# Optimization experiments

Measured on AMD Instinct MI355X. Metric: run time of the kernel, lower is better.

## Reference

```python
import jax, jax.numpy as jnp
import numpy as np

SMOOTH_STEP_PARAM = 1.0  # = 1/gamma in the TEL paper
DEPTH = 6


def smooth_step(x):
    # TEL smooth-step: 0 for u<=-1/2, 1 for u>=1/2, cubic -2u^3+1.5u+0.5 inside.
    u = SMOOTH_STEP_PARAM * x
    inner = (-2.0 * u + 1.5) * u * u + (u + 0.5) * 0.0 + (-2.0 * u ** 3 + 1.5 * u + 0.5)
    # use single clean expression for the cubic
    cubic = -2.0 * u ** 3 + 1.5 * u + 0.5
    return jnp.where(u <= -0.5, 0.0, jnp.where(u >= 0.5, 1.0, cubic))


def setup_inputs() -> dict:
    key = jax.random.key(0)
    k1, k2, k3 = jax.random.split(key, 3)
    B, D, T, O = 32768, 1024, 8, 128
    num_leaves = 2 ** DEPTH
    x = jax.random.normal(k1, (B, D), dtype=jnp.float32)
    # RandomUniform(-0.01, 0.01) initializers in the original layer
    node_weights = jax.random.uniform(k2, (T, D, num_leaves - 1), dtype=jnp.float32,
                                      minval=-0.01, maxval=0.01)
    leaf_weights = jax.random.uniform(k3, (T, O, num_leaves), dtype=jnp.float32,
                                      minval=-0.01, maxval=0.01)
    return {"x": x, "node_weights": node_weights, "leaf_weights": leaf_weights}


def reference(x, node_weights, leaf_weights):
    B = x.shape[0]
    T = node_weights.shape[0]
    # routing probabilities at every internal node (BFS order): [B, T, 2^depth-1]
    s = smooth_step(jnp.einsum('bd,tdi->bti', x, node_weights))
    # accumulate leaf reach probabilities level by level (left child gets s)
    mu = jnp.ones((B, T, 1), dtype=x.dtype)
    start = 0
    for level in range(DEPTH):
        width = 2 ** level
        s_lvl = s[:, :, start:start + width]           # [B, T, width]
        mu = jnp.stack([mu * s_lvl, mu * (1.0 - s_lvl)], axis=-1)
        mu = mu.reshape(B, T, 2 * width)
        start += width
    # weighted sum of leaf vectors, summed over trees (sum_outputs=True)
    return jnp.einsum('btl,tol->bo', mu, leaf_weights)
```

## Files before the change

kernel.cpp:

```cpp
#include <hip/hip_runtime.h>
#include <hip/hip_bf16.h>
#include <stdint.h>

#define KDIM 1024
#define TSTR 72
#define RSTR 576

typedef __attribute__((ext_vector_type(4))) float f32x4;
typedef __attribute__((ext_vector_type(8))) short bf16x8;

#define WS_LB_OFF ((size_t)1 << 20)

__device__ __forceinline__ unsigned short f2bf_rne(float f) {
    unsigned u = __float_as_uint(f);
    u = (u + 0x7fffu + ((u >> 16) & 1u)) >> 16;
    return (unsigned short)u;
}

__device__ __forceinline__ unsigned int pack2_bf16(float a, float b) {
    __hip_bfloat162 h = __float22bfloat162_rn(make_float2(a, b));
    union { __hip_bfloat162 h; unsigned int u; } cv;
    cv.h = h;
    return cv.u;
}

__device__ __forceinline__ float gs_get(const uint4* q, int i) {
    uint4 v = q[i >> 3];
    int c = (i >> 1) & 3;
    unsigned w = (c == 0) ? v.x : (c == 1) ? v.y : (c == 2) ? v.z : v.w;
    return __uint_as_float((i & 1) ? (w & 0xffff0000u) : (w << 16));
}

__global__ void prep_w(const float* __restrict__ nw, unsigned short* __restrict__ wb) {
    int idx = blockIdx.x * 256 + threadIdx.x;
    int kl = idx & 31;
    int n  = (idx >> 5) & 511;
    int ks = idx >> 14;
    int cp = kl >> 3, e = kl & 7;
    int kchunk = cp ^ (n & 3);
    int d = ks * 32 + kchunk * 8 + e;
    int t = n >> 6, i = n & 63;
    float v = (i < 63) ? nw[(t * KDIM + d) * 63 + i] : 0.0f;
    wb[idx] = f2bf_rne(v);
}

__global__ void prep_l(const float* __restrict__ lw, unsigned short* __restrict__ lb) {
    int idx = blockIdx.x * 256 + threadIdx.x;
    int kk = idx & 31;
    int o  = (idx >> 5) & 127;
    int kq = idx >> 12;
    int c = kq * 32 + kk;
    int t = c >> 6, l = c & 63;
    lb[idx] = f2bf_rne(lw[(t * 128 + o) * 64 + l]);
}

__launch_bounds__(256, 2)
__global__ void fused(const float* __restrict__ x, const unsigned short* __restrict__ wb,
                      const unsigned short* __restrict__ lb, float* __restrict__ out) {
    __shared__ union __align__(16) {
        struct {
            unsigned short xs[64 * 40];
            unsigned short wl[512 * 32];
        } k;
        unsigned short st[32 * RSTR];
    } sm;

    const int tid  = threadIdx.x;
    const int wave = tid >> 6, lane = tid & 63;
    const int quad = lane >> 4, l16 = lane & 15;
    const int mb   = blockIdx.x;

    f32x4 acc[8][4];
    const f32x4 z4 = {0.f, 0.f, 0.f, 0.f};
    #pragma unroll
    for (int a = 0; a < 8; ++a)
        #pragma unroll
        for (int b = 0; b < 4; ++b) acc[a][b] = z4;

    const int xrow = tid >> 2, xq = tid & 3;
    const float* xg0 = x + (size_t)(mb * 64 + xrow) * KDIM + xq * 8;

    for (int ks = 0; ks < 32; ++ks) {
        __syncthreads();
        const unsigned short* wks = wb + (size_t)ks * (512 * 32);
        #pragma unroll
        for (int it = 0; it < 8; ++it) {
            const unsigned short* gp = wks + (size_t)(it * 256 + tid) * 8;
            __builtin_amdgcn_global_load_lds(
                (const __attribute__((address_space(1))) unsigned int*)gp,
                (__attribute__((address_space(3))) unsigned int*)&sm.k.wl[(it * 256 + wave * 64) * 8],
                16, 0, 0);
        }
        {
            const float4* xg = (const float4*)(xg0 + ks * 32);
            float4 f0 = xg[0], f1 = xg[1];
            uint4 p;
            p.x = pack2_bf16(f0.x, f0.y); p.y = pack2_bf16(f0.z, f0.w);
            p.z = pack2_bf16(f1.x, f1.y); p.w = pack2_bf16(f1.z, f1.w);
            *(uint4*)&sm.k.xs[xrow * 40 + xq * 8] = p;
        }
        __syncthreads();
        bf16x8 af[8], bf[4];
        #pragma unroll
        for (int ct = 0; ct < 8; ++ct) {
            int col = wave * 128 + ct * 16 + l16;
            int chunk = quad ^ (col & 3);
            af[ct] = *(const bf16x8*)&sm.k.wl[col * 32 + chunk * 8];
        }
        #pragma unroll
        for (int rt = 0; rt < 4; ++rt)
            bf[rt] = *(const bf16x8*)&sm.k.xs[(rt * 16 + l16) * 40 + quad * 8];
        #pragma unroll
        for (int ct = 0; ct < 8; ++ct)
            #pragma unroll
            for (int rt = 0; rt < 4; ++rt)
                acc[ct][rt] = __builtin_amdgcn_mfma_f32_16x16x32_bf16(af[ct], bf[rt], acc[ct][rt], 0, 0, 0);
    }

    #pragma unroll
    for (int p = 0; p < 2; ++p) {
        __syncthreads();
        #pragma unroll
        for (int rt2 = 0; rt2 < 2; ++rt2) {
            int rowl = rt2 * 16 + l16;
            #pragma unroll
            for (int ct = 0; ct < 8; ++ct) {
                int colb = wave * 128 + ct * 16 + quad * 4;
                f32x4 a = acc[ct][p * 2 + rt2];
                float s0[4];
                #pragma unroll
                for (int j = 0; j < 4; ++j) {
                    float u = a[j];
                    u = fminf(fmaxf(u, -0.5f), 0.5f);
                    s0[j] = u * (1.5f - 2.0f * u * u) + 0.5f;
                }
                uint2 pk;
                pk.x = pack2_bf16(s0[0], s0[1]);
                pk.y = pack2_bf16(s0[2], s0[3]);
                *(uint2*)&sm.st[rowl * RSTR + (colb >> 6) * TSTR + (colb & 63)] = pk;
            }
        }
        __syncthreads();
        {
            int r = tid >> 3, t = tid & 7;
            unsigned short* base = &sm.st[r * RSTR + t * TSTR];
            uint4 q[8];
            #pragma unroll
            for (int c = 0; c < 8; ++c) q[c] = *(const uint4*)(base + c * 8);
            float mu[32];
            mu[0] = 1.0f;
            int start = 0;
            #pragma unroll
            for (int lvl = 0; lvl < 5; ++lvl) {
                int width = 1 << lvl;
                #pragma unroll
                for (int j = width - 1; j >= 0; --j) {
                    float m = mu[j], s_ = gs_get(q, start + j);
                    mu[2 * j + 1] = m * (1.0f - s_);
                    mu[2 * j]     = m * s_;
                }
                start += width;
            }
            #pragma unroll
            for (int c = 0; c < 8; ++c) {
                unsigned pk2[4];
                #pragma unroll
                for (int e = 0; e < 4; ++e) {
                    int j = c * 4 + e;
                    float m = mu[j], s_ = gs_get(q, 31 + j);
                    pk2[e] = pack2_bf16(m * s_, m * (1.0f - s_));
                }
                uint4 v; v.x = pk2[0]; v.y = pk2[1]; v.z = pk2[2]; v.w = pk2[3];
                *(uint4*)(base + c * 8) = v;
            }
        }
        __syncthreads();
        {
            int rtile = wave & 1, ob = (wave >> 1) * 64;
            f32x4 a2[4];
            a2[0] = z4; a2[1] = z4; a2[2] = z4; a2[3] = z4;
            #pragma unroll
            for (int kq = 0; kq < 16; ++kq) {
                int c0 = kq * 32 + quad * 8;
                bf16x8 bmu = *(const bf16x8*)&sm.st[(rtile * 16 + l16) * RSTR + (c0 >> 6) * TSTR + (c0 & 63)];
                #pragma unroll
                for (int ct = 0; ct < 4; ++ct) {
                    int o = ob + ct * 16 + l16;
                    bf16x8 alf = *(const bf16x8*)(lb + (size_t)(kq * 128 + o) * 32 + quad * 8);
                    a2[ct] = __builtin_amdgcn_mfma_f32_16x16x32_bf16(alf, bmu, a2[ct], 0, 0, 0);
                }
            }
            #pragma unroll
            for (int ct = 0; ct < 4; ++ct) {
                int rowg = mb * 64 + p * 32 + rtile * 16 + l16;
                int og = ob + ct * 16 + quad * 4;
                *(f32x4*)(out + (size_t)rowg * 128 + og) = a2[ct];
            }
        }
    }
}

extern "C" void kernel_launch(void* const* d_in, const int* in_sizes, int n_in,
                              void* d_out, int out_size, void* d_ws, size_t ws_size,
                              hipStream_t stream) {
    const float* x  = (const float*)d_in[0];
    const float* nw = (const float*)d_in[1];
    const float* lw = (const float*)d_in[2];
    float* out = (float*)d_out;

    unsigned short* wb = (unsigned short*)d_ws;
    unsigned short* lb = (unsigned short*)((char*)d_ws + WS_LB_OFF);

    prep_w<<<2048, 256, 0, stream>>>(nw, wb);
    prep_l<<<256, 256, 0, stream>>>(lw, lb);
    fused<<<512, 256, 0, stream>>>(x, wb, lb, out);
}
```

Before: 240.6 us.

## Halve row tile to 32 and stage weights through registers instead of direct LDS loads

The fused kernel now processes 32 batch rows per block instead of 64, launching 1024 blocks, which removes the two-pass epilogue loop. Weight tiles are loaded through registers into LDS with regular vector stores, replacing global_load_lds, and the shared-memory union is split into separate arrays. This trades more total weight traffic per row (each weight tile is reused over fewer rows) and more LDS use per block for more parallelism and a simpler epilogue.

```diff
diff --git a/kernel.cpp b/kernel.cpp
--- a/kernel.cpp
+++ b/kernel.cpp
@@ -57,145 +57,140 @@
 __launch_bounds__(256, 2)
 __global__ void fused(const float* __restrict__ x, const unsigned short* __restrict__ wb,
                       const unsigned short* __restrict__ lb, float* __restrict__ out) {
-    __shared__ union __align__(16) {
-        struct {
-            unsigned short xs[64 * 40];
-            unsigned short wl[512 * 32];
-        } k;
-        unsigned short st[32 * RSTR];
-    } sm;
+    __shared__ __align__(16) unsigned short xs[32 * 40];
+    __shared__ __align__(16) unsigned short wl[512 * 32];
+    __shared__ __align__(16) unsigned short st[32 * RSTR];
 
     const int tid  = threadIdx.x;
     const int wave = tid >> 6, lane = tid & 63;
     const int quad = lane >> 4, l16 = lane & 15;
     const int mb   = blockIdx.x;
 
-    f32x4 acc[8][4];
+    f32x4 acc[8][2];
     const f32x4 z4 = {0.f, 0.f, 0.f, 0.f};
     #pragma unroll
-    for (int a = 0; a < 8; ++a)
-        #pragma unroll
-        for (int b = 0; b < 4; ++b) acc[a][b] = z4;
-
-    const int xrow = tid >> 2, xq = tid & 3;
-    const float* xg0 = x + (size_t)(mb * 64 + xrow) * KDIM + xq * 8;
+    for (int a = 0; a < 8; ++a) { acc[a][0] = z4; acc[a][1] = z4; }
+
+    const int xrow = tid >> 3, xq8 = tid & 7;
+    const float* xg0 = x + (size_t)(mb * 32 + xrow) * KDIM + xq8 * 4;
 
     for (int ks = 0; ks < 32; ++ks) {
+        __threadfence_block();
         __syncthreads();
         const unsigned short* wks = wb + (size_t)ks * (512 * 32);
         #pragma unroll
-        for (int it = 0; it < 8; ++it) {
-            const unsigned short* gp = wks + (size_t)(it * 256 + tid) * 8;
-            __builtin_amdgcn_global_load_lds(
-                (const __attribute__((address_space(1))) unsigned int*)gp,
-                (__attribute__((address_space(3))) unsigned int*)&sm.k.wl[(it * 256 + wave * 64) * 8],
-                16, 0, 0);
+        for (int h = 0; h < 2; ++h) {
+            uint4 wv[4];
+            #pragma unroll
+            for (int it = 0; it < 4; ++it)
+                wv[it] = *(const uint4*)(wks + (size_t)((h * 4 + it) * 256 + tid) * 8);
+            #pragma unroll
+            for (int it = 0; it < 4; ++it)
+                *(uint4*)&wl[((h * 4 + it) * 256 + tid) * 8] = wv[it];
         }
         {
-            const float4* xg = (const float4*)(xg0 + ks * 32);
-            float4 f0 = xg[0], f1 = xg[1];
-            uint4 p;
-            p.x = pack2_bf16(f0.x, f0.y); p.y = pack2_bf16(f0.z, f0.w);
-            p.z = pack2_bf16(f1.x, f1.y); p.w = pack2_bf16(f1.z, f1.w);
-            *(uint4*)&sm.k.xs[xrow * 40 + xq * 8] = p;
-        }
+            float4 f0 = *(const float4*)(xg0 + ks * 32);
+            uint2 pk;
+            pk.x = pack2_bf16(f0.x, f0.y);
+            pk.y = pack2_bf16(f0.z, f0.w);
+            *(uint2*)&xs[xrow * 40 + xq8 * 4] = pk;
+        }
+        __threadfence_block();
         __syncthreads();
-        bf16x8 af[8], bf[4];
+        bf16x8 af[8], bfr[2];
         #pragma unroll
         for (int ct = 0; ct < 8; ++ct) {
             int col = wave * 128 + ct * 16 + l16;
             int chunk = quad ^ (col & 3);
-            af[ct] = *(const bf16x8*)&sm.k.wl[col * 32 + chunk * 8];
-        }
-        #pragma unroll
-        for (int rt = 0; rt < 4; ++rt)
-            bf[rt] = *(const bf16x8*)&sm.k.xs[(rt * 16 + l16) * 40 + quad * 8];
+            af[ct] = *(const bf16x8*)&wl[col * 32 + chunk * 8];
+        }
+        #pragma unroll
+        for (int rt = 0; rt < 2; ++rt)
+            bfr[rt] = *(const bf16x8*)&xs[(rt * 16 + l16) * 40 + quad * 8];
         #pragma unroll
         for (int ct = 0; ct < 8; ++ct)
             #pragma unroll
-            for (int rt = 0; rt < 4; ++rt)
-                acc[ct][rt] = __builtin_amdgcn_mfma_f32_16x16x32_bf16(af[ct], bf[rt], acc[ct][rt], 0, 0, 0);
-    }
-
+            for (int rt = 0; rt < 2; ++rt)
+                acc[ct][rt] = __builtin_amdgcn_mfma_f32_16x16x32_bf16(af[ct], bfr[rt], acc[ct][rt], 0, 0, 0);
+    }
+
+    __threadfence_block();
+    __syncthreads();
     #pragma unroll
-    for (int p = 0; p < 2; ++p) {
-        __syncthreads();
-        #pragma unroll
-        for (int rt2 = 0; rt2 < 2; ++rt2) {
-            int rowl = rt2 * 16 + l16;
-            #pragma unroll
-            for (int ct = 0; ct < 8; ++ct) {
-                int colb = wave * 128 + ct * 16 + quad * 4;
-                f32x4 a = acc[ct][p * 2 + rt2];
-                float s0[4];
-                #pragma unroll
-                for (int j = 0; j < 4; ++j) {
-                    float u = a[j];
-                    u = fminf(fmaxf(u, -0.5f), 0.5f);
-                    s0[j] = u * (1.5f - 2.0f * u * u) + 0.5f;
-                }
-                uint2 pk;
-                pk.x = pack2_bf16(s0[0], s0[1]);
-                pk.y = pack2_bf16(s0[2], s0[3]);
-                *(uint2*)&sm.st[rowl * RSTR + (colb >> 6) * TSTR + (colb & 63)] = pk;
-            }
-        }
-        __syncthreads();
-        {
-            int r = tid >> 3, t = tid & 7;
-            unsigned short* base = &sm.st[r * RSTR + t * TSTR];
-            uint4 q[8];
-            #pragma unroll
-            for (int c = 0; c < 8; ++c) q[c] = *(const uint4*)(base + c * 8);
-            float mu[32];
-            mu[0] = 1.0f;
-            int start = 0;
-            #pragma unroll
-            for (int lvl = 0; lvl < 5; ++lvl) {
-                int width = 1 << lvl;
-                #pragma unroll
-                for (int j = width - 1; j >= 0; --j) {
-                    float m = mu[j], s_ = gs_get(q, start + j);
-                    mu[2 * j + 1] = m * (1.0f - s_);
-                    mu[2 * j]     = m * s_;
-                }
-                start += width;
-            }
-            #pragma unroll
-            for (int c = 0; c < 8; ++c) {
-                unsigned pk2[4];
-                #pragma unroll
-                for (int e = 0; e < 4; ++e) {
-                    int j = c * 4 + e;
-                    float m = mu[j], s_ = gs_get(q, 31 + j);
-                    pk2[e] = pack2_bf16(m * s_, m * (1.0f - s_));
-                }
-                uint4 v; v.x = pk2[0]; v.y = pk2[1]; v.z = pk2[2]; v.w = pk2[3];
-                *(uint4*)(base + c * 8) = v;
-            }
-        }
-        __syncthreads();
-        {
-            int rtile = wave & 1, ob = (wave >> 1) * 64;
-            f32x4 a2[4];
-            a2[0] = z4; a2[1] = z4; a2[2] = z4; a2[3] = z4;
-            #pragma unroll
-            for (int kq = 0; kq < 16; ++kq) {
-                int c0 = kq * 32 + quad * 8;
-                bf16x8 bmu = *(const bf16x8*)&sm.st[(rtile * 16 + l16) * RSTR + (c0 >> 6) * TSTR + (c0 & 63)];
-                #pragma unroll
-                for (int ct = 0; ct < 4; ++ct) {
-                    int o = ob + ct * 16 + l16;
-                    bf16x8 alf = *(const bf16x8*)(lb + (size_t)(kq * 128 + o) * 32 + quad * 8);
-                    a2[ct] = __builtin_amdgcn_mfma_f32_16x16x32_bf16(alf, bmu, a2[ct], 0, 0, 0);
-                }
-            }
+    for (int rt2 = 0; rt2 < 2; ++rt2) {
+        int row = rt2 * 16 + l16;
+        #pragma unroll
+        for (int ct = 0; ct < 8; ++ct) {
+            int colb = wave * 128 + ct * 16 + quad * 4;
+            f32x4 a = acc[ct][rt2];
+            float s0[4];
+            #pragma unroll
+            for (int j = 0; j < 4; ++j) {
+                float u = a[j];
+                u = fminf(fmaxf(u, -0.5f), 0.5f);
+                s0[j] = u * (1.5f - 2.0f * u * u) + 0.5f;
+            }
+            uint2 pk;
+            pk.x = pack2_bf16(s0[0], s0[1]);
+            pk.y = pack2_bf16(s0[2], s0[3]);
+            *(uint2*)&st[row * RSTR + (colb >> 6) * TSTR + (colb & 63)] = pk;
+        }
+    }
+    __syncthreads();
+    {
+        int r = tid >> 3, t = tid & 7;
+        unsigned short* base = &st[r * RSTR + t * TSTR];
+        uint4 q[8];
+        #pragma unroll
+        for (int c = 0; c < 8; ++c) q[c] = *(const uint4*)(base + c * 8);
+        float mu[32];
+        mu[0] = 1.0f;
+        int start = 0;
+        #pragma unroll
+        for (int lvl = 0; lvl < 5; ++lvl) {
+            int width = 1 << lvl;
+            #pragma unroll
+            for (int j = width - 1; j >= 0; --j) {
+                float m = mu[j], s_ = gs_get(q, start + j);
+                mu[2 * j + 1] = m * (1.0f - s_);
+                mu[2 * j]     = m * s_;
+            }
+            start += width;
+        }
+        #pragma unroll
+        for (int c = 0; c < 8; ++c) {
+            unsigned pk2[4];
+            #pragma unroll
+            for (int e = 0; e < 4; ++e) {
+                int j = c * 4 + e;
+                float m = mu[j], s_ = gs_get(q, 31 + j);
+                pk2[e] = pack2_bf16(m * s_, m * (1.0f - s_));
+            }
+            uint4 v; v.x = pk2[0]; v.y = pk2[1]; v.z = pk2[2]; v.w = pk2[3];
+            *(uint4*)(base + c * 8) = v;
+        }
+    }
+    __syncthreads();
+    {
+        int rtile = wave & 1, ob = (wave >> 1) * 64;
+        f32x4 a2[4];
+        a2[0] = z4; a2[1] = z4; a2[2] = z4; a2[3] = z4;
+        #pragma unroll
+        for (int kq = 0; kq < 16; ++kq) {
+            int c0 = kq * 32 + quad * 8;
+            bf16x8 bmu = *(const bf16x8*)&st[(rtile * 16 + l16) * RSTR + (c0 >> 6) * TSTR + (c0 & 63)];
             #pragma unroll
             for (int ct = 0; ct < 4; ++ct) {
-                int rowg = mb * 64 + p * 32 + rtile * 16 + l16;
-                int og = ob + ct * 16 + quad * 4;
-                *(f32x4*)(out + (size_t)rowg * 128 + og) = a2[ct];
-            }
+                int o = ob + ct * 16 + l16;
+                bf16x8 alf = *(const bf16x8*)(lb + (size_t)(kq * 128 + o) * 32 + quad * 8);
+                a2[ct] = __builtin_amdgcn_mfma_f32_16x16x32_bf16(alf, bmu, a2[ct], 0, 0, 0);
+            }
+        }
+        #pragma unroll
+        for (int ct = 0; ct < 4; ++ct) {
+            int rowg = mb * 32 + rtile * 16 + l16;
+            int og = ob + ct * 16 + quad * 4;
+            *(f32x4*)(out + (size_t)rowg * 128 + og) = a2[ct];
         }
     }
 }
@@ -213,5 +208,5 @@
 
     prep_w<<<2048, 256, 0, stream>>>(nw, wb);
     prep_l<<<256, 256, 0, stream>>>(lw, lb);
-    fused<<<512, 256, 0, stream>>>(x, wb, lb, out);
-}
+    fused<<<1024, 256, 0, stream>>>(x, wb, lb, out);
+}
```

Measured after the change: 273.4 us. +13.6%, slower.
